# Kernel tuning notes

Measured on AMD Instinct MI355X. Metric: run time of the kernel, lower is better.

Reference implementation:

```python
import jax, jax.numpy as jnp
import numpy as np

B = 4096
T_STEPS = 2048


def setup_inputs() -> dict:
    key = jax.random.key(0)
    k1, k2, k3 = jax.random.split(key, 3)
    inputs = jax.random.normal(k1, (B, T_STEPS), dtype=jnp.float32)
    # replicate torch init: params = rand(t); params /= sum(|params|); alternate signs
    p = jax.random.uniform(k2, (T_STEPS,), dtype=jnp.float32)
    p = p / jnp.sum(jnp.abs(p))
    sign = jnp.where(jnp.arange(T_STEPS) % 2 == 0, jnp.float32(1.0), jnp.float32(-1.0))
    params = p * sign
    bias = jax.random.normal(k3, (1,), dtype=jnp.float32)
    return {"inputs": inputs, "params": params, "bias": bias}


def reference(inputs, params, bias):
    """AR(t) recurrence: for i in [t, 2t): x_i = sum_j x_{i-1-j} * params[j] + bias.
    inputs: [B, t] seed values; returns the t generated values per row, [B, t].
    """
    t_steps = params.shape[0]
    # torch.dot uses inputs reversed (newest first) against params, so the
    # window kept in oldest->newest order pairs with reversed params.
    p_rev = params[::-1]

    def step(window, _):
        # window: [B, t] last t values, oldest -> newest
        new = window @ p_rev + bias[0]  # [B]
        window = jnp.concatenate([window[:, 1:], new[:, None]], axis=1)
        return window, new

    _, outs = jax.lax.scan(step, inputs, None, length=t_steps)
    return outs.T  # [B, t_steps]
```

## Files before the change

kernel.cpp:

```cpp
#include <hip/hip_runtime.h>
#include <hip/hip_bf16.h>

typedef _Float16 f16;
typedef _Float16 f16x8 __attribute__((ext_vector_type(8)));
typedef float f32x4 __attribute__((ext_vector_type(4)));

constexpr int TS = 2048;
constexpr int BB = 4096;

struct ToepShared { char Xs[16384]; char Ws[8192]; };

struct __align__(16) HShared {
  float rq[2048];
  float h[2048];
  float histp_store[2048];
  float part_buf[4096];
};

template <bool REV>
__device__ void toep_body(ToepShared& lds, int w, const f16* __restrict__ Xg,
                          const char* __restrict__ Wg,
                          const float* __restrict__ biasp, void* __restrict__ Yg) {
  char* Xs = lds.Xs;
  char* Ws = lds.Ws;
  const int tid = threadIdx.x;
  const int lane = tid & 63;
  const int wid = tid >> 6;
  const int wrow = (wid >> 1) * 64;
  const int wcol = (wid & 1) * 32;
  const int px = w & 15;
  const int b0 = (w >> 4) * 128;

  float binit = 0.0f;
  if (REV) binit = biasp[0];

  for (int phase = 0; phase < 2; ++phase) {
    const int mblk = phase ? (31 - px) : px;
    const int m0 = mblk * 64;
    const int k0b = REV ? m0 : 0;
    const int k0e = REV ? TS : (m0 + 64);

    f32x4 acc[4][2];
    #pragma unroll
    for (int i = 0; i < 4; ++i)
      #pragma unroll
      for (int j = 0; j < 2; ++j) acc[i][j] = {binit, binit, binit, binit};

    for (int k0 = k0b; k0 < k0e; k0 += 64) {
      __syncthreads();
      #pragma unroll
      for (int t2 = 0; t2 < 4; ++t2) {
        const int t = wid * 4 + t2;
        const int row = t * 8 + (lane >> 3);
        const char* src = (const char*)Xg + ((size_t)(b0 + row) * TS + k0) * 2
                          + (((lane & 7) * 16) ^ ((row & 7) << 4));
        __builtin_amdgcn_global_load_lds(
            (const __attribute__((address_space(1))) unsigned int*)src,
            (__attribute__((address_space(3))) unsigned int*)(Xs + t * 1024),
            16, 0, 0);
      }
      const int dlt = (REV ? (k0 - m0) : (m0 - k0)) >> 6;
      const char* wsrc = Wg + (size_t)dlt * 8192;
      #pragma unroll
      for (int p = 0; p < 2; ++p) {
        const int t = wid * 2 + p;
        __builtin_amdgcn_global_load_lds(
            (const __attribute__((address_space(1))) unsigned int*)(wsrc + t * 1024 + lane * 16),
            (__attribute__((address_space(3))) unsigned int*)(Ws + t * 1024),
            16, 0, 0);
      }
      __syncthreads();

      #pragma unroll
      for (int ks = 0; ks < 2; ++ks) {
        const int colb = ks * 64 + ((lane >> 4) * 16);
        f16x8 af[4], bf[2];
        #pragma unroll
        for (int i = 0; i < 4; ++i) {
          const int row = wrow + i * 16 + (lane & 15);
          af[i] = *(const f16x8*)(Xs + row * 128 + (colb ^ ((row & 7) << 4)));
        }
        #pragma unroll
        for (int j = 0; j < 2; ++j) {
          const int n = wcol + j * 16 + (lane & 15);
          bf[j] = *(const f16x8*)(Ws + n * 128 + (colb ^ ((n & 7) << 4)));
        }
        #pragma unroll
        for (int i = 0; i < 4; ++i)
          #pragma unroll
          for (int j = 0; j < 2; ++j)
            acc[i][j] = __builtin_amdgcn_mfma_f32_16x16x32_f16(
                af[i], bf[j], acc[i][j], 0, 0, 0);
      }
    }

    #pragma unroll
    for (int i = 0; i < 4; ++i) {
      #pragma unroll
      for (int j = 0; j < 2; ++j) {
        #pragma unroll
        for (int r = 0; r < 4; ++r) {
          const int row = b0 + wrow + i * 16 + (lane >> 4) * 4 + r;
          const int col = m0 + wcol + j * 16 + (lane & 15);
          if (REV)
            ((f16*)Yg)[(size_t)row * TS + col] = (f16)acc[i][j][r];
          else
            ((float*)Yg)[(size_t)row * TS + col] = acc[i][j][r];
        }
      }
    }
  }
}

__device__ void h_block_body(HShared& S, const float* __restrict__ params,
                             char* __restrict__ WgC) {
  float* rq = S.rq;
  float* h_s = S.h;
  float* histp = S.histp_store + 1024;
  const int tid = threadIdx.x;
  const int lane = tid & 63;
  const int wave = tid >> 6;

  if (tid < 512) {
    f32x4 pv = *(const f32x4*)&params[2044 - 4 * tid];
    f32x4 v = {pv[3], pv[2], pv[1], pv[0]};
    *(f32x4*)&rq[4 * tid] = v;
  }
  if (tid < 256) {
    f32x4 z = {0.0f, 0.0f, 0.0f, 0.0f};
    *(f32x4*)&S.histp_store[4 * tid] = z;
  }
  __syncthreads();

  if (wave == 0) {
    float hv = (lane == 0) ? 1.0f : 0.0f;
    for (int m = 1; m < 32; ++m) {
      float partial = (lane < m) ? hv * rq[2048 - m + lane] : 0.0f;
      #pragma unroll
      for (int off = 32; off; off >>= 1) partial += __shfl_xor(partial, off);
      if (lane == m) hv = partial;
    }
    if (lane < 32) h_s[lane] = hv;
  }
  __syncthreads();

  #pragma unroll 1
  for (int n = 32; n < 2048; n <<= 1) {
    int NC = n >> 8; if (NC < 1) NC = 1;
    int SPLIT = 16 / NC;
    if (SPLIT > (n >> 2)) SPLIT = n >> 2;
    const int part = n / SPLIT;
    const int T = part >> 2;
    const int c = wave % NC;
    const int s = wave / NC;
    const int iB = c * 256 + (lane << 2);
    const int m0 = s * part;
    const bool act = (s < SPLIT) && (iB < n);

    if (act) {
      float a0 = 0.0f, a1 = 0.0f, a2 = 0.0f, a3 = 0.0f;
      const float* wp = &rq[2048 - n - iB + m0];
      f32x4 prev = *(const f32x4*)(wp - 4);
      for (int t = 0; t < T; ++t) {
        const f32x4 lo = prev;
        const f32x4 hi = *(const f32x4*)(wp + 4 * t);
        const f32x4 h4 = *(const f32x4*)&h_s[m0 + 4 * t];
        a0 += h4[0] * hi[0] + h4[1] * hi[1] + h4[2] * hi[2] + h4[3] * hi[3];
        a1 += h4[0] * lo[3] + h4[1] * hi[0] + h4[2] * hi[1] + h4[3] * hi[2];
        a2 += h4[0] * lo[2] + h4[1] * lo[3] + h4[2] * hi[0] + h4[3] * hi[1];
        a3 += h4[0] * lo[1] + h4[1] * lo[2] + h4[2] * lo[3] + h4[3] * hi[0];
        prev = hi;
      }
      f32x4 out = {a0, a1, a2, a3};
      *(f32x4*)&S.part_buf[s * n + iB] = out;
    }
    __syncthreads();
    if (tid < n) {
      float v = 0.0f;
      for (int s2 = 0; s2 < SPLIT; ++s2) v += S.part_buf[s2 * n + tid];
      histp[tid] = v;
    }
    __syncthreads();

    if (act) {
      int wmax = c * 256 + 255; if (wmax > n - 1) wmax = n - 1;
      int T2 = ((wmax - m0) >> 2) + 1;
      if (T2 > T) T2 = T;
      if (T2 < 0) T2 = 0;
      float a0 = 0.0f, a1 = 0.0f, a2 = 0.0f, a3 = 0.0f;
      const float* hp = &histp[iB - m0];
      f32x4 hi = *(const f32x4*)hp;
      for (int t = 0; t < T2; ++t) {
        const f32x4 lo = *(const f32x4*)(hp - 4 - 4 * t);
        const f32x4 h4 = *(const f32x4*)&h_s[m0 + 4 * t];
        a0 += h4[0] * hi[0] + h4[1] * lo[3] + h4[2] * lo[2] + h4[3] * lo[1];
        a1 += h4[0] * hi[1] + h4[1] * hi[0] + h4[2] * lo[3] + h4[3] * lo[2];
        a2 += h4[0] * hi[2] + h4[1] * hi[1] + h4[2] * hi[0] + h4[3] * lo[3];
        a3 += h4[0] * hi[3] + h4[1] * hi[2] + h4[2] * hi[1] + h4[3] * hi[0];
        hi = lo;
      }
      f32x4 out = {a0, a1, a2, a3};
      *(f32x4*)&S.part_buf[s * n + iB] = out;
    }
    __syncthreads();
    if (tid < n) {
      float v = 0.0f;
      for (int s2 = 0; s2 < SPLIT; ++s2) v += S.part_buf[s2 * n + tid];
      h_s[n + tid] = v;
    }
    __syncthreads();
  }

  const int kq = (tid >> 6) & 3;
  const int n2 = tid & 63;
  for (int dlt = tid >> 8; dlt < 32; dlt += 4) {
    char* tile = WgC + (size_t)dlt * 8192;
    #pragma unroll
    for (int part2 = 0; part2 < 2; ++part2) {
      const int k8 = kq * 16 + part2 * 8;
      f16x8 v;
      #pragma unroll
      for (int ii = 0; ii < 8; ++ii) {
        const int dd = dlt * 64 + n2 - (k8 + ii);
        v[ii] = ((unsigned)dd < (unsigned)TS) ? (f16)h_s[dd] : (f16)0.0f;
      }
      *(f16x8*)(tile + n2 * 128 + ((2 * k8) ^ ((n2 & 7) << 4))) = v;
    }
  }
}

__global__ __launch_bounds__(1024, 1) void conv_prep(
    const float* __restrict__ X, f16* __restrict__ Xh,
    const float* __restrict__ params, char* __restrict__ Wg) {
  __shared__ HShared S;
  const int b = blockIdx.x;
  const int tid = threadIdx.x;

  if (b == 0) {
    h_block_body(S, params, Wg + 32 * 8192);
    return;
  }
  if (b <= 8) {
    const int dlt = (b - 1) * 4 + (tid >> 8);
    char* tile = Wg + (size_t)dlt * 8192;
    const int s2 = tid & 255;
    const int n = s2 >> 2, kq = s2 & 3;
    #pragma unroll
    for (int part = 0; part < 2; ++part) {
      const int k8 = kq * 16 + part * 8;
      f16x8 v;
      #pragma unroll
      for (int ii = 0; ii < 8; ++ii) {
        const int k = k8 + ii;
        const int dd = dlt * 64 + k - n;
        v[ii] = ((unsigned)dd < (unsigned)TS) ? (f16)params[2047 - dd] : (f16)0.0f;
      }
      *(f16x8*)(tile + n * 128 + ((2 * k8) ^ ((n & 7) << 4))) = v;
    }
    return;
  }
  const size_t base = ((size_t)(b - 9) * 1024 + tid) * 16;
  const float4 a0 = *(const float4*)&X[base];
  const float4 a1 = *(const float4*)&X[base + 4];
  const float4 a2 = *(const float4*)&X[base + 8];
  const float4 a3 = *(const float4*)&X[base + 12];
  f16x8 v0 = {(f16)a0.x, (f16)a0.y, (f16)a0.z, (f16)a0.w,
              (f16)a1.x, (f16)a1.y, (f16)a1.z, (f16)a1.w};
  f16x8 v1 = {(f16)a2.x, (f16)a2.y, (f16)a2.z, (f16)a2.w,
              (f16)a3.x, (f16)a3.y, (f16)a3.z, (f16)a3.w};
  *(f16x8*)&Xh[base] = v0;
  *(f16x8*)&Xh[base + 8] = v1;
}

__global__ __launch_bounds__(256, 2) void toep_A(
    const f16* __restrict__ Xh, const char* __restrict__ Wg,
    const float* __restrict__ biasp, f16* __restrict__ u) {
  __shared__ ToepShared lds;
  const int b = blockIdx.x;
  toep_body<true>(lds, (b & 7) * 64 + (b >> 3), Xh, Wg, biasp, (void*)u);
}

__global__ __launch_bounds__(256, 2) void toep_C(
    const f16* __restrict__ u, const char* __restrict__ WgC,
    float* __restrict__ out) {
  __shared__ ToepShared lds;
  const int b = blockIdx.x;
  toep_body<false>(lds, (b & 7) * 64 + (b >> 3), u, WgC, nullptr, (void*)out);
}

extern "C" void kernel_launch(void* const* d_in, const int* in_sizes, int n_in,
                              void* d_out, int out_size, void* d_ws, size_t ws_size,
                              hipStream_t stream) {
  const float* inputs = (const float*)d_in[0];
  const float* params = (const float*)d_in[1];
  const float* bias   = (const float*)d_in[2];
  float* out = (float*)d_out;

  char* ws = (char*)d_ws;
  f16*  Xh = (f16*)ws;
  f16*  u  = (f16*)(ws + (size_t)BB * TS * 2);
  char* Wg = ws + (size_t)BB * TS * 4;

  conv_prep<<<521, 1024, 0, stream>>>(inputs, Xh, params, Wg);
  toep_A<<<512, 256, 0, stream>>>(Xh, Wg, bias, u);
  toep_C<<<512, 256, 0, stream>>>(u, Wg + 32 * 8192, out);
}
```

Before: 107.7 us.

## Split last impulse-response doubling step across extra blocks and defer WgC build

Result: faster. 95.50 us (-11.3%).

```diff
diff --git a/kernel.cpp b/kernel.cpp
--- a/kernel.cpp
+++ b/kernel.cpp
@@ -113,7 +113,7 @@
 }
 
 __device__ void h_block_body(HShared& S, const float* __restrict__ params,
-                             char* __restrict__ WgC) {
+                             float* __restrict__ h_g) {
   float* rq = S.rq;
   float* h_s = S.h;
   float* histp = S.histp_store + 1024;
@@ -145,7 +145,7 @@
   __syncthreads();
 
   #pragma unroll 1
-  for (int n = 32; n < 2048; n <<= 1) {
+  for (int n = 32; n < 1024; n <<= 1) {
     int NC = n >> 8; if (NC < 1) NC = 1;
     int SPLIT = 16 / NC;
     if (SPLIT > (n >> 2)) SPLIT = n >> 2;
@@ -211,33 +211,106 @@
     __syncthreads();
   }
 
-  const int kq = (tid >> 6) & 3;
-  const int n2 = tid & 63;
-  for (int dlt = tid >> 8; dlt < 32; dlt += 4) {
-    char* tile = WgC + (size_t)dlt * 8192;
-    #pragma unroll
-    for (int part2 = 0; part2 < 2; ++part2) {
-      const int k8 = kq * 16 + part2 * 8;
-      f16x8 v;
-      #pragma unroll
-      for (int ii = 0; ii < 8; ++ii) {
-        const int dd = dlt * 64 + n2 - (k8 + ii);
-        v[ii] = ((unsigned)dd < (unsigned)TS) ? (f16)h_s[dd] : (f16)0.0f;
-      }
-      *(f16x8*)(tile + n2 * 128 + ((2 * k8) ^ ((n2 & 7) << 4))) = v;
-    }
-  }
+  if (tid < 256) *(f32x4*)&h_g[4 * tid] = *(const f32x4*)&h_s[4 * tid];
+}
+
+__global__ __launch_bounds__(256, 1) void h_H1024(
+    const float* __restrict__ params, const float* __restrict__ h_g,
+    float* __restrict__ hist_g) {
+  __shared__ __align__(16) float rq[2048];
+  __shared__ __align__(16) float hl[1024];
+  __shared__ __align__(16) float part[1024];
+  const int tid = threadIdx.x;
+  const int lane = tid & 63;
+  const int wave = tid >> 6;
+  const int B = blockIdx.x;
+
+  for (int c = tid; c < 512; c += 256) {
+    f32x4 pv = *(const f32x4*)&params[2044 - 4 * c];
+    f32x4 v = {pv[3], pv[2], pv[1], pv[0]};
+    *(f32x4*)&rq[4 * c] = v;
+  }
+  *(f32x4*)&hl[4 * tid] = *(const f32x4*)&h_g[4 * tid];
+  __syncthreads();
+
+  const int iB = B * 256 + (lane << 2);
+  const int m0 = wave * 256;
+  float a0 = 0.0f, a1 = 0.0f, a2 = 0.0f, a3 = 0.0f;
+  const float* wp = &rq[1024 - iB + m0];
+  f32x4 prev = *(const f32x4*)(wp - 4);
+  #pragma unroll 4
+  for (int t = 0; t < 64; ++t) {
+    const f32x4 lo = prev;
+    const f32x4 hi = *(const f32x4*)(wp + 4 * t);
+    const f32x4 h4 = *(const f32x4*)&hl[m0 + 4 * t];
+    a0 += h4[0] * hi[0] + h4[1] * hi[1] + h4[2] * hi[2] + h4[3] * hi[3];
+    a1 += h4[0] * lo[3] + h4[1] * hi[0] + h4[2] * hi[1] + h4[3] * hi[2];
+    a2 += h4[0] * lo[2] + h4[1] * lo[3] + h4[2] * hi[0] + h4[3] * hi[1];
+    a3 += h4[0] * lo[1] + h4[1] * lo[2] + h4[2] * lo[3] + h4[3] * hi[0];
+    prev = hi;
+  }
+  f32x4 out = {a0, a1, a2, a3};
+  *(f32x4*)&part[wave * 256 + (lane << 2)] = out;
+  __syncthreads();
+  const float v = (part[tid] + part[256 + tid]) + (part[512 + tid] + part[768 + tid]);
+  hist_g[B * 256 + tid] = v;
+}
+
+__global__ __launch_bounds__(256, 1) void h_S1024(
+    const float* __restrict__ hist_g, float* __restrict__ h_g) {
+  __shared__ __align__(16) float hps[2048];
+  __shared__ __align__(16) float hl[1024];
+  __shared__ __align__(16) float part[1024];
+  const int tid = threadIdx.x;
+  const int lane = tid & 63;
+  const int wave = tid >> 6;
+  const int B = blockIdx.x;
+
+  {
+    f32x4 z = {0.0f, 0.0f, 0.0f, 0.0f};
+    *(f32x4*)&hps[4 * tid] = z;
+    *(f32x4*)&hps[1024 + 4 * tid] = *(const f32x4*)&hist_g[4 * tid];
+    *(f32x4*)&hl[4 * tid] = *(const f32x4*)&h_g[4 * tid];
+  }
+  __syncthreads();
+
+  float* histp = hps + 1024;
+  const int iB = B * 256 + (lane << 2);
+  const int m0 = wave * 256;
+  const int wmax = B * 256 + 255;
+  int T2 = 0;
+  if (wmax >= m0) { T2 = ((wmax - m0) >> 2) + 1; if (T2 > 64) T2 = 64; }
+
+  float a0 = 0.0f, a1 = 0.0f, a2 = 0.0f, a3 = 0.0f;
+  const float* hp = &histp[iB - m0];
+  f32x4 hi = *(const f32x4*)hp;
+  #pragma unroll 4
+  for (int t = 0; t < T2; ++t) {
+    const f32x4 lo = *(const f32x4*)(hp - 4 - 4 * t);
+    const f32x4 h4 = *(const f32x4*)&hl[m0 + 4 * t];
+    a0 += h4[0] * hi[0] + h4[1] * lo[3] + h4[2] * lo[2] + h4[3] * lo[1];
+    a1 += h4[0] * hi[1] + h4[1] * hi[0] + h4[2] * lo[3] + h4[3] * lo[2];
+    a2 += h4[0] * hi[2] + h4[1] * hi[1] + h4[2] * hi[0] + h4[3] * lo[3];
+    a3 += h4[0] * hi[3] + h4[1] * hi[2] + h4[2] * hi[1] + h4[3] * hi[0];
+    hi = lo;
+  }
+  f32x4 out = {a0, a1, a2, a3};
+  *(f32x4*)&part[wave * 256 + (lane << 2)] = out;
+  __syncthreads();
+  const float v = (part[tid] + part[256 + tid]) + (part[512 + tid] + part[768 + tid]);
+  h_g[1024 + B * 256 + tid] = v;
 }
 
 __global__ __launch_bounds__(1024, 1) void conv_prep(
     const float* __restrict__ X, f16* __restrict__ Xh,
-    const float* __restrict__ params, char* __restrict__ Wg) {
+    const float* __restrict__ params, char* __restrict__ Wg,
+    float* __restrict__ h_g) {
   __shared__ HShared S;
   const int b = blockIdx.x;
   const int tid = threadIdx.x;
 
   if (b == 0) {
-    h_block_body(S, params, Wg + 32 * 8192);
+    h_block_body(S, params, h_g);
     return;
   }
   if (b <= 8) {
@@ -274,9 +347,31 @@
 
 __global__ __launch_bounds__(256, 2) void toep_A(
     const f16* __restrict__ Xh, const char* __restrict__ Wg,
-    const float* __restrict__ biasp, f16* __restrict__ u) {
+    const float* __restrict__ biasp, f16* __restrict__ u,
+    const float* __restrict__ h_g, char* __restrict__ WgC) {
   __shared__ ToepShared lds;
   const int b = blockIdx.x;
+  if (b >= 512) {
+    const int bw = b - 512;
+    const int tid = threadIdx.x;
+    const int kq = tid >> 6;
+    const int n2 = tid & 63;
+    for (int dlt = bw * 8; dlt < bw * 8 + 8; ++dlt) {
+      char* tile = WgC + (size_t)dlt * 8192;
+      #pragma unroll
+      for (int part = 0; part < 2; ++part) {
+        const int k8 = kq * 16 + part * 8;
+        f16x8 v;
+        #pragma unroll
+        for (int ii = 0; ii < 8; ++ii) {
+          const int dd = dlt * 64 + n2 - (k8 + ii);
+          v[ii] = ((unsigned)dd < (unsigned)TS) ? (f16)h_g[dd] : (f16)0.0f;
+        }
+        *(f16x8*)(tile + n2 * 128 + ((2 * k8) ^ ((n2 & 7) << 4))) = v;
+      }
+    }
+    return;
+  }
   toep_body<true>(lds, (b & 7) * 64 + (b >> 3), Xh, Wg, biasp, (void*)u);
 }
 
@@ -297,11 +392,15 @@
   float* out = (float*)d_out;
 
   char* ws = (char*)d_ws;
-  f16*  Xh = (f16*)ws;
-  f16*  u  = (f16*)(ws + (size_t)BB * TS * 2);
-  char* Wg = ws + (size_t)BB * TS * 4;
-
-  conv_prep<<<521, 1024, 0, stream>>>(inputs, Xh, params, Wg);
-  toep_A<<<512, 256, 0, stream>>>(Xh, Wg, bias, u);
+  f16*   Xh    = (f16*)ws;
+  f16*   u     = (f16*)(ws + (size_t)BB * TS * 2);
+  char*  Wg    = ws + (size_t)BB * TS * 4;
+  float* h_g   = (float*)(Wg + 64 * 8192);
+  float* hist_g = h_g + 2048;
+
+  conv_prep<<<521, 1024, 0, stream>>>(inputs, Xh, params, Wg, h_g);
+  h_H1024<<<4, 256, 0, stream>>>(params, h_g, hist_g);
+  h_S1024<<<4, 256, 0, stream>>>(hist_g, h_g);
+  toep_A<<<516, 256, 0, stream>>>(Xh, Wg, bias, u, h_g, Wg + 32 * 8192);
   toep_C<<<512, 256, 0, stream>>>(u, Wg + 32 * 8192, out);
 }
```

## Offload C-tile construction from serial h block to extra toep_A blocks

Applied to the files above, without the earlier changes.

Result: faster. 104.3 us (-3.2%).

```diff
diff --git a/kernel.cpp b/kernel.cpp
--- a/kernel.cpp
+++ b/kernel.cpp
@@ -113,7 +113,7 @@
 }
 
 __device__ void h_block_body(HShared& S, const float* __restrict__ params,
-                             char* __restrict__ WgC) {
+                             float* __restrict__ h_g) {
   float* rq = S.rq;
   float* h_s = S.h;
   float* histp = S.histp_store + 1024;
@@ -175,10 +175,11 @@
       *(f32x4*)&S.part_buf[s * n + iB] = out;
     }
     __syncthreads();
-    if (tid < n) {
-      float v = 0.0f;
-      for (int s2 = 0; s2 < SPLIT; ++s2) v += S.part_buf[s2 * n + tid];
-      histp[tid] = v;
+    if (tid < (n >> 2)) {
+      f32x4 v = {0.0f, 0.0f, 0.0f, 0.0f};
+      for (int s2 = 0; s2 < SPLIT; ++s2)
+        v += *(const f32x4*)&S.part_buf[s2 * n + 4 * tid];
+      *(f32x4*)&histp[4 * tid] = v;
     }
     __syncthreads();
 
@@ -203,41 +204,28 @@
       *(f32x4*)&S.part_buf[s * n + iB] = out;
     }
     __syncthreads();
-    if (tid < n) {
-      float v = 0.0f;
-      for (int s2 = 0; s2 < SPLIT; ++s2) v += S.part_buf[s2 * n + tid];
-      h_s[n + tid] = v;
+    if (tid < (n >> 2)) {
+      f32x4 v = {0.0f, 0.0f, 0.0f, 0.0f};
+      for (int s2 = 0; s2 < SPLIT; ++s2)
+        v += *(const f32x4*)&S.part_buf[s2 * n + 4 * tid];
+      *(f32x4*)&h_s[n + 4 * tid] = v;
     }
     __syncthreads();
   }
 
-  const int kq = (tid >> 6) & 3;
-  const int n2 = tid & 63;
-  for (int dlt = tid >> 8; dlt < 32; dlt += 4) {
-    char* tile = WgC + (size_t)dlt * 8192;
-    #pragma unroll
-    for (int part2 = 0; part2 < 2; ++part2) {
-      const int k8 = kq * 16 + part2 * 8;
-      f16x8 v;
-      #pragma unroll
-      for (int ii = 0; ii < 8; ++ii) {
-        const int dd = dlt * 64 + n2 - (k8 + ii);
-        v[ii] = ((unsigned)dd < (unsigned)TS) ? (f16)h_s[dd] : (f16)0.0f;
-      }
-      *(f16x8*)(tile + n2 * 128 + ((2 * k8) ^ ((n2 & 7) << 4))) = v;
-    }
-  }
+  if (tid < 512) *(f32x4*)&h_g[4 * tid] = *(const f32x4*)&h_s[4 * tid];
 }
 
 __global__ __launch_bounds__(1024, 1) void conv_prep(
     const float* __restrict__ X, f16* __restrict__ Xh,
-    const float* __restrict__ params, char* __restrict__ Wg) {
+    const float* __restrict__ params, char* __restrict__ Wg,
+    float* __restrict__ h_g) {
   __shared__ HShared S;
   const int b = blockIdx.x;
   const int tid = threadIdx.x;
 
   if (b == 0) {
-    h_block_body(S, params, Wg + 32 * 8192);
+    h_block_body(S, params, h_g);
     return;
   }
   if (b <= 8) {
@@ -274,9 +262,31 @@
 
 __global__ __launch_bounds__(256, 2) void toep_A(
     const f16* __restrict__ Xh, const char* __restrict__ Wg,
-    const float* __restrict__ biasp, f16* __restrict__ u) {
+    const float* __restrict__ biasp, f16* __restrict__ u,
+    const float* __restrict__ h_g, char* __restrict__ WgC) {
   __shared__ ToepShared lds;
   const int b = blockIdx.x;
+  if (b >= 512) {
+    const int bw = b - 512;
+    const int tid = threadIdx.x;
+    const int kq = tid >> 6;
+    const int n2 = tid & 63;
+    for (int dlt = bw * 8; dlt < bw * 8 + 8; ++dlt) {
+      char* tile = WgC + (size_t)dlt * 8192;
+      #pragma unroll
+      for (int part = 0; part < 2; ++part) {
+        const int k8 = kq * 16 + part * 8;
+        f16x8 v;
+        #pragma unroll
+        for (int ii = 0; ii < 8; ++ii) {
+          const int dd = dlt * 64 + n2 - (k8 + ii);
+          v[ii] = ((unsigned)dd < (unsigned)TS) ? (f16)h_g[dd] : (f16)0.0f;
+        }
+        *(f16x8*)(tile + n2 * 128 + ((2 * k8) ^ ((n2 & 7) << 4))) = v;
+      }
+    }
+    return;
+  }
   toep_body<true>(lds, (b & 7) * 64 + (b >> 3), Xh, Wg, biasp, (void*)u);
 }
 
@@ -297,11 +307,12 @@
   float* out = (float*)d_out;
 
   char* ws = (char*)d_ws;
-  f16*  Xh = (f16*)ws;
-  f16*  u  = (f16*)(ws + (size_t)BB * TS * 2);
-  char* Wg = ws + (size_t)BB * TS * 4;
-
-  conv_prep<<<521, 1024, 0, stream>>>(inputs, Xh, params, Wg);
-  toep_A<<<512, 256, 0, stream>>>(Xh, Wg, bias, u);
+  f16*   Xh  = (f16*)ws;
+  f16*   u   = (f16*)(ws + (size_t)BB * TS * 2);
+  char*  Wg  = ws + (size_t)BB * TS * 4;
+  float* h_g = (float*)(Wg + 64 * 8192);
+
+  conv_prep<<<521, 1024, 0, stream>>>(inputs, Xh, params, Wg, h_g);
+  toep_A<<<516, 256, 0, stream>>>(Xh, Wg, bias, u, h_g, Wg + 32 * 8192);
   toep_C<<<512, 256, 0, stream>>>(u, Wg + 32 * 8192, out);
 }
```
